# Performance work log

Measured on AMD Instinct MI355X. Metric: run time of the kernel, lower is better.

Reference implementation:

```python
import jax, jax.numpy as jnp
import numpy as np

IGNORE_INDEX = 255
THRESH = 0.7
MIN_KEPT = 100000


def _ohem_ce(predict, target):
    # predict: (n, c, h, w) float logits; target: (n, h, w) int labels
    n, c, h, w = predict.shape
    logits = predict.transpose(0, 2, 3, 1).reshape(-1, c)   # (P, c), P = n*h*w
    labels = target.reshape(-1)                              # (P,)

    valid = labels != IGNORE_INDEX
    safe_labels = jnp.where(valid, labels, 0)

    # stable log-softmax once; prob-at-label = exp(logp-at-label)
    logp = jax.nn.log_softmax(logits, axis=-1)               # (P, c)
    logp_lab = jnp.take_along_axis(logp, safe_labels[:, None], axis=-1)[:, 0]  # (P,)
    pred = jnp.exp(logp_lab)                                 # softmax prob of true class

    num_valid = jnp.sum(valid)

    # k-th smallest prob among valid pixels (selection is not differentiated,
    # matching the torch code which does this on numpy/CPU)
    pred_ng = jax.lax.stop_gradient(pred)
    pred_sel = jnp.where(valid, pred_ng, jnp.inf)
    neg_topk, _ = jax.lax.top_k(-pred_sel, MIN_KEPT)         # MIN_KEPT smallest preds
    kth = -neg_topk[-1]                                      # MIN_KEPT-th smallest

    threshold = jnp.where(kth > THRESH, kth, THRESH)

    # OHEM keep rule only applies when num_valid > min_kept; otherwise keep all valid
    do_ohem = num_valid > MIN_KEPT
    kept = jnp.where(do_ohem, valid & (pred_ng <= threshold), valid)

    cnt = jnp.sum(kept)
    # CrossEntropyLoss(mean over non-ignored) on kept pixels
    loss = -jnp.sum(jnp.where(kept, logp_lab, 0.0)) / jnp.maximum(cnt, 1).astype(logp_lab.dtype)
    return loss


def setup_inputs() -> dict:
    key = jax.random.key(0)
    k1, k2 = jax.random.split(key)
    predict = jax.random.normal(k1, (8, 19, 512, 1024), dtype=jnp.float32)
    target = jax.random.randint(k2, (8, 512, 1024), 0, 19, dtype=jnp.int64)
    return {"predict": predict, "target": target}


def reference(predict, target):
    return _ohem_ce(predict, target)
```

## Files before the change

kernel.cpp:

```cpp
#include <hip/hip_runtime.h>
#include <cfloat>
#include <math.h>

#define P_TOT     4194304
#define HW_       524288
#define NCLS      19
#define IGNORE_IDX 255
#define MIN_KEPT_ 100000
#define NBLK      4096
#define THR       0.7f
#define L2E       1.44269504088896340736f
#define LN2       0.69314718055994530942f

__device__ __forceinline__ double wred_d(double v){
  #pragma unroll
  for (int o = 32; o > 0; o >>= 1) v += __shfl_down(v, o, 64);
  return v;
}
__device__ __forceinline__ unsigned wred_u(unsigned v){
  #pragma unroll
  for (int o = 32; o > 0; o >>= 1) v += __shfl_down(v, o, 64);
  return v;
}

__global__ __launch_bounds__(256) void ohem_pass1(
    const float* __restrict__ logits, const int* __restrict__ tgt,
    double* __restrict__ p_sle, double* __restrict__ p_sva,
    unsigned* __restrict__ p_cnt)
{
  int tid = blockIdx.x * 256 + threadIdx.x;
  int p0  = tid * 4;
  int n   = p0 >> 19;
  int r   = p0 & (HW_ - 1);
  const float* base = logits + (size_t)n * (NCLS * (size_t)HW_) + r;

  int4 tl = *(const int4*)(tgt + p0);
  int q0 = (tl.x != IGNORE_IDX), q1 = (tl.y != IGNORE_IDX);
  int q2 = (tl.z != IGNORE_IDX), q3 = (tl.w != IGNORE_IDX);
  int l0 = q0 ? tl.x : 0, l1 = q1 ? tl.y : 0;
  int l2 = q2 ? tl.z : 0, l3 = q3 ? tl.w : 0;

  float g0 = base[(size_t)l0 * HW_ + 0];
  float g1 = base[(size_t)l1 * HW_ + 1];
  float g2 = base[(size_t)l2 * HW_ + 2];
  float g3 = base[(size_t)l3 * HW_ + 3];

  float4 vals[NCLS];
  float4 mx; mx.x = mx.y = mx.z = mx.w = -FLT_MAX;
  #pragma unroll
  for (int c = 0; c < NCLS; c++){
    float4 v = *(const float4*)(base + (size_t)c * HW_);
    vals[c] = v;
    mx.x = fmaxf(mx.x, v.x); mx.y = fmaxf(mx.y, v.y);
    mx.z = fmaxf(mx.z, v.z); mx.w = fmaxf(mx.w, v.w);
  }
  float4 nm;
  nm.x = -mx.x * L2E; nm.y = -mx.y * L2E;
  nm.z = -mx.z * L2E; nm.w = -mx.w * L2E;
  float4 se; se.x = se.y = se.z = se.w = 0.f;
  #pragma unroll
  for (int c = 0; c < NCLS; c++){
    se.x += exp2f(fmaf(vals[c].x, L2E, nm.x));
    se.y += exp2f(fmaf(vals[c].y, L2E, nm.y));
    se.z += exp2f(fmaf(vals[c].z, L2E, nm.z));
    se.w += exp2f(fmaf(vals[c].w, L2E, nm.w));
  }

  float lp0 = (g0 - mx.x) - log2f(se.x) * LN2;
  float lp1 = (g1 - mx.y) - log2f(se.y) * LN2;
  float lp2 = (g2 - mx.z) - log2f(se.z) * LN2;
  float lp3 = (g3 - mx.w) - log2f(se.w) * LN2;
  float pd0 = __expf(lp0), pd1 = __expf(lp1);
  float pd2 = __expf(lp2), pd3 = __expf(lp3);

  double sle = 0.0, sva = 0.0;
  unsigned cnt = 0;
  #define PIXEL(Q, LP, PD) {                                   \
    if (Q){                                                    \
      cnt += 1u; sva += (double)(LP);                          \
      if ((PD) <= THR){ cnt += 1u << 16; sle += (double)(LP); }\
    }                                                          \
  }
  PIXEL(q0, lp0, pd0) PIXEL(q1, lp1, pd1)
  PIXEL(q2, lp2, pd2) PIXEL(q3, lp3, pd3)
  #undef PIXEL

  sle = wred_d(sle); sva = wred_d(sva); cnt = wred_u(cnt);

  __shared__ double  ls1[4], ls2[4];
  __shared__ unsigned lc[4];
  int wv = threadIdx.x >> 6, ln = threadIdx.x & 63;
  if (ln == 0){ ls1[wv] = sle; ls2[wv] = sva; lc[wv] = cnt; }
  __syncthreads();
  if (threadIdx.x == 0){
    p_sle[blockIdx.x] = ls1[0] + ls1[1] + ls1[2] + ls1[3];
    p_sva[blockIdx.x] = ls2[0] + ls2[1] + ls2[2] + ls2[3];
    p_cnt[blockIdx.x] = lc[0] + lc[1] + lc[2] + lc[3];
  }
}

__global__ __launch_bounds__(1024) void ohem_finish(
    const float* __restrict__ logits, const int* __restrict__ tgt,
    const double* __restrict__ p_sle, const double* __restrict__ p_sva,
    const unsigned* __restrict__ p_cnt,
    unsigned* __restrict__ keys, float* __restrict__ logp,
    float* __restrict__ out)
{
  __shared__ double  rs1[16], rs2[16];
  __shared__ unsigned rc1[16], rc2[16];
  __shared__ unsigned s_flag, s_prefix, s_rank;
  __shared__ unsigned s_hist[4096];

  int t = threadIdx.x;
  double sle = 0.0, sva = 0.0; unsigned cle = 0, cva = 0;
  for (int i = t; i < NBLK; i += 1024){
    sle += p_sle[i]; sva += p_sva[i];
    unsigned c = p_cnt[i];
    cva += c & 0xFFFFu; cle += c >> 16;
  }
  sle = wred_d(sle); sva = wred_d(sva);
  cle = wred_u(cle); cva = wred_u(cva);
  int wv = t >> 6, ln = t & 63;
  if (ln == 0){ rs1[wv] = sle; rs2[wv] = sva; rc1[wv] = cle; rc2[wv] = cva; }
  __syncthreads();
  if (t == 0){
    double S1 = 0, S2 = 0; unsigned C1 = 0, C2 = 0;
    for (int i = 0; i < 16; i++){ S1 += rs1[i]; S2 += rs2[i]; C1 += rc1[i]; C2 += rc2[i]; }
    unsigned flag;
    if (C2 <= MIN_KEPT_){
      unsigned d = C2 > 1u ? C2 : 1u;
      out[0] = (float)(-S2 / (double)d);
      flag = 0;
    } else if (C1 >= MIN_KEPT_){
      out[0] = (float)(-S1 / (double)C1);
      flag = 0;
    } else flag = 1;
    s_flag = flag;
  }
  __syncthreads();
  if (!s_flag) return;

  for (int p = t; p < P_TOT; p += 1024){
    int n = p >> 19; int r = p & (HW_ - 1);
    const float* bp = logits + (size_t)n * (NCLS * (size_t)HW_) + r;
    int lab = tgt[p];
    int lv  = (lab != IGNORE_IDX);
    int ls  = lv ? lab : 0;
    float mxv = -FLT_MAX, va[NCLS];
    #pragma unroll
    for (int c = 0; c < NCLS; c++){
      float x = bp[(size_t)c * HW_];
      va[c] = x; mxv = fmaxf(mxv, x);
    }
    float xlv = va[0];
    #pragma unroll
    for (int c = 1; c < NCLS; c++) if (c == ls) xlv = va[c];
    float sev = 0.f;
    #pragma unroll
    for (int c = 0; c < NCLS; c++) sev += __expf(va[c] - mxv);
    float lp = (xlv - mxv) - __logf(sev);
    float pd = __expf(lp);
    keys[p] = lv ? __float_as_uint(pd) : 0xFFFFFFFFu;
    logp[p] = lp;
  }
  __syncthreads();

  unsigned prefix = 0, rank = MIN_KEPT_;
  #pragma unroll
  for (int rd = 0; rd < 3; rd++){
    const int sh = (rd == 0) ? 20 : (rd == 1) ? 8 : 0;
    const int nb = (rd == 2) ? 8 : 12;
    const unsigned nbin = 1u << nb;
    for (unsigned i = t; i < nbin; i += 1024) s_hist[i] = 0;
    __syncthreads();
    for (int p = t; p < P_TOT; p += 1024){
      unsigned k = keys[p];
      unsigned hi = (rd == 0) ? 0u : (k >> (sh + nb));
      if (hi == prefix) atomicAdd(&s_hist[(k >> sh) & (nbin - 1)], 1u);
    }
    __syncthreads();
    if (t == 0){
      unsigned cum = 0, b = 0;
      for (; b < nbin - 1; b++){
        unsigned cc = s_hist[b];
        if (cum + cc >= rank) break;
        cum += cc;
      }
      s_prefix = (prefix << nb) | b;
      s_rank = rank - cum;
    }
    __syncthreads();
    prefix = s_prefix; rank = s_rank;
    __syncthreads();
  }
  unsigned kb = prefix;

  double s = 0.0; unsigned c = 0;
  for (int p = t; p < P_TOT; p += 1024){
    unsigned k = keys[p];
    if (k <= kb){ c++; s += (double)logp[p]; }
  }
  s = wred_d(s); c = wred_u(c);
  if (ln == 0){ rs1[wv] = s; rc1[wv] = c; }
  __syncthreads();
  if (t == 0){
    double S = 0; unsigned CC = 0;
    for (int i = 0; i < 16; i++){ S += rs1[i]; CC += rc1[i]; }
    unsigned d = CC > 1u ? CC : 1u;
    out[0] = (float)(-S / (double)d);
  }
}

extern "C" void kernel_launch(void* const* d_in, const int* in_sizes, int n_in,
                              void* d_out, int out_size, void* d_ws, size_t ws_size,
                              hipStream_t stream)
{
  const float* logits = (const float*)d_in[0];
  const int*   tgt    = (const int*)d_in[1];
  float* out = (float*)d_out;

  double*   p_sle = (double*)d_ws;
  double*   p_sva = p_sle + NBLK;
  unsigned* p_cnt = (unsigned*)(p_sva + NBLK);
  unsigned* keys  = p_cnt + NBLK;
  float*    logp  = (float*)(keys + P_TOT);

  hipLaunchKernelGGL(ohem_pass1, dim3(NBLK), dim3(256), 0, stream,
                     logits, tgt, p_sle, p_sva, p_cnt);
  hipLaunchKernelGGL(ohem_finish, dim3(1), dim3(1024), 0, stream,
                     logits, tgt, p_sle, p_sva, p_cnt, keys, logp, out);
}
```

Before: 439.3 us.

## Stream logits via double-buffered global_load_lds DMA in persistent single-wave blocks

Pass 1 now launches 1024 single-wave blocks. Each block walks 16 consecutive 256-pixel tiles and prefetches the next tile's 19 class planes and labels into LDS with global_load_lds, double-buffered and ordered by explicit waitcnt. The label-class gather now reads from LDS instead of issuing extra scattered global loads, and the exp/log calls use the raw hardware builtins. The aim is to overlap memory latency with compute on a bandwidth-bound read of about 320MB. The cost is far fewer concurrent waves (1024 wave64s across the GPU), which may not saturate HBM, and the hand-coded waitcnt immediates carry a correctness risk.

```diff
diff --git a/kernel.cpp b/kernel.cpp
--- a/kernel.cpp
+++ b/kernel.cpp
@@ -1,16 +1,26 @@
 #include <hip/hip_runtime.h>
 #include <cfloat>
-#include <math.h>
+#include <stdint.h>
 
 #define P_TOT     4194304
 #define HW_       524288
 #define NCLS      19
 #define IGNORE_IDX 255
 #define MIN_KEPT_ 100000
-#define NBLK      4096
 #define THR       0.7f
 #define L2E       1.44269504088896340736f
 #define LN2       0.69314718055994530942f
+
+#define NWAVE          1024
+#define TILES_PER_WAVE 16
+#define TILE_PX        256
+#define BUF_BYTES      20480
+
+__device__ __forceinline__ void dma16(const void* g, void* l){
+  __builtin_amdgcn_global_load_lds(
+      (const __attribute__((address_space(1))) uint32_t*)g,
+      (__attribute__((address_space(3))) uint32_t*)l, 16, 0, 0);
+}
 
 __device__ __forceinline__ double wred_d(double v){
   #pragma unroll
@@ -23,79 +33,102 @@
   return v;
 }
 
-__global__ __launch_bounds__(256) void ohem_pass1(
+__global__ __launch_bounds__(64) void ohem_pass1(
     const float* __restrict__ logits, const int* __restrict__ tgt,
     double* __restrict__ p_sle, double* __restrict__ p_sva,
     unsigned* __restrict__ p_cnt)
 {
-  int tid = blockIdx.x * 256 + threadIdx.x;
-  int p0  = tid * 4;
-  int n   = p0 >> 19;
-  int r   = p0 & (HW_ - 1);
-  const float* base = logits + (size_t)n * (NCLS * (size_t)HW_) + r;
-
-  int4 tl = *(const int4*)(tgt + p0);
-  int q0 = (tl.x != IGNORE_IDX), q1 = (tl.y != IGNORE_IDX);
-  int q2 = (tl.z != IGNORE_IDX), q3 = (tl.w != IGNORE_IDX);
-  int l0 = q0 ? tl.x : 0, l1 = q1 ? tl.y : 0;
-  int l2 = q2 ? tl.z : 0, l3 = q3 ? tl.w : 0;
-
-  float g0 = base[(size_t)l0 * HW_ + 0];
-  float g1 = base[(size_t)l1 * HW_ + 1];
-  float g2 = base[(size_t)l2 * HW_ + 2];
-  float g3 = base[(size_t)l3 * HW_ + 3];
-
-  float4 vals[NCLS];
-  float4 mx; mx.x = mx.y = mx.z = mx.w = -FLT_MAX;
-  #pragma unroll
-  for (int c = 0; c < NCLS; c++){
-    float4 v = *(const float4*)(base + (size_t)c * HW_);
-    vals[c] = v;
-    mx.x = fmaxf(mx.x, v.x); mx.y = fmaxf(mx.y, v.y);
-    mx.z = fmaxf(mx.z, v.z); mx.w = fmaxf(mx.w, v.w);
-  }
-  float4 nm;
-  nm.x = -mx.x * L2E; nm.y = -mx.y * L2E;
-  nm.z = -mx.z * L2E; nm.w = -mx.w * L2E;
-  float4 se; se.x = se.y = se.z = se.w = 0.f;
-  #pragma unroll
-  for (int c = 0; c < NCLS; c++){
-    se.x += exp2f(fmaf(vals[c].x, L2E, nm.x));
-    se.y += exp2f(fmaf(vals[c].y, L2E, nm.y));
-    se.z += exp2f(fmaf(vals[c].z, L2E, nm.z));
-    se.w += exp2f(fmaf(vals[c].w, L2E, nm.w));
-  }
-
-  float lp0 = (g0 - mx.x) - log2f(se.x) * LN2;
-  float lp1 = (g1 - mx.y) - log2f(se.y) * LN2;
-  float lp2 = (g2 - mx.z) - log2f(se.z) * LN2;
-  float lp3 = (g3 - mx.w) - log2f(se.w) * LN2;
-  float pd0 = __expf(lp0), pd1 = __expf(lp1);
-  float pd2 = __expf(lp2), pd3 = __expf(lp3);
+  __shared__ uint8_t lds[2 * BUF_BYTES];
+  const int lane = threadIdx.x;
+  const int t0   = blockIdx.x * TILES_PER_WAVE;
+
+  {
+    int p0 = t0 * TILE_PX;
+    int n = p0 >> 19, r0 = p0 & (HW_ - 1);
+    const float* pb = logits + (size_t)n * (NCLS * (size_t)HW_) + r0 + lane * 4;
+    #pragma unroll
+    for (int c = 0; c < NCLS; c++)
+      dma16(pb + (size_t)c * HW_, &lds[c * 1024]);
+    dma16(tgt + p0 + lane * 4, &lds[19 * 1024]);
+  }
 
   double sle = 0.0, sva = 0.0;
   unsigned cnt = 0;
-  #define PIXEL(Q, LP, PD) {                                   \
-    if (Q){                                                    \
-      cnt += 1u; sva += (double)(LP);                          \
-      if ((PD) <= THR){ cnt += 1u << 16; sle += (double)(LP); }\
-    }                                                          \
-  }
-  PIXEL(q0, lp0, pd0) PIXEL(q1, lp1, pd1)
-  PIXEL(q2, lp2, pd2) PIXEL(q3, lp3, pd3)
-  #undef PIXEL
+
+  for (int i = 0; i < TILES_PER_WAVE; i++){
+    const uint8_t* buf = &lds[(i & 1) * BUF_BYTES];
+
+    if (i + 1 < TILES_PER_WAVE){
+      int p0 = (t0 + i + 1) * TILE_PX;
+      int n = p0 >> 19, r0 = p0 & (HW_ - 1);
+      const float* pb = logits + (size_t)n * (NCLS * (size_t)HW_) + r0 + lane * 4;
+      uint8_t* nbuf = &lds[((i + 1) & 1) * BUF_BYTES];
+      #pragma unroll
+      for (int c = 0; c < NCLS; c++)
+        dma16(pb + (size_t)c * HW_, nbuf + c * 1024);
+      dma16(tgt + p0 + lane * 4, nbuf + 19 * 1024);
+      __builtin_amdgcn_s_waitcnt(0x4F74);
+    } else {
+      __builtin_amdgcn_s_waitcnt(0x0F70);
+    }
+
+    int4 tl = *((const int4*)(buf + 19 * 1024) + lane);
+
+    float4 vals[NCLS];
+    float4 mx; mx.x = mx.y = mx.z = mx.w = -FLT_MAX;
+    #pragma unroll
+    for (int c = 0; c < NCLS; c++){
+      float4 v = *((const float4*)(buf + c * 1024) + lane);
+      vals[c] = v;
+      mx.x = fmaxf(mx.x, v.x); mx.y = fmaxf(mx.y, v.y);
+      mx.z = fmaxf(mx.z, v.z); mx.w = fmaxf(mx.w, v.w);
+    }
+    float4 nm;
+    nm.x = -mx.x * L2E; nm.y = -mx.y * L2E;
+    nm.z = -mx.z * L2E; nm.w = -mx.w * L2E;
+    float4 se; se.x = se.y = se.z = se.w = 0.f;
+    #pragma unroll
+    for (int c = 0; c < NCLS; c++){
+      se.x += __builtin_amdgcn_exp2f(fmaf(vals[c].x, L2E, nm.x));
+      se.y += __builtin_amdgcn_exp2f(fmaf(vals[c].y, L2E, nm.y));
+      se.z += __builtin_amdgcn_exp2f(fmaf(vals[c].z, L2E, nm.z));
+      se.w += __builtin_amdgcn_exp2f(fmaf(vals[c].w, L2E, nm.w));
+    }
+
+    int q0 = (tl.x != IGNORE_IDX), q1 = (tl.y != IGNORE_IDX);
+    int q2 = (tl.z != IGNORE_IDX), q3 = (tl.w != IGNORE_IDX);
+    int l0 = q0 ? tl.x : 0, l1 = q1 ? tl.y : 0;
+    int l2 = q2 ? tl.z : 0, l3 = q3 ? tl.w : 0;
+    float g0 = *(const float*)(buf + l0 * 1024 + lane * 16 + 0);
+    float g1 = *(const float*)(buf + l1 * 1024 + lane * 16 + 4);
+    float g2 = *(const float*)(buf + l2 * 1024 + lane * 16 + 8);
+    float g3 = *(const float*)(buf + l3 * 1024 + lane * 16 + 12);
+
+    float lp0 = (g0 - mx.x) - __builtin_amdgcn_logf(se.x) * LN2;
+    float lp1 = (g1 - mx.y) - __builtin_amdgcn_logf(se.y) * LN2;
+    float lp2 = (g2 - mx.z) - __builtin_amdgcn_logf(se.z) * LN2;
+    float lp3 = (g3 - mx.w) - __builtin_amdgcn_logf(se.w) * LN2;
+    float pd0 = __builtin_amdgcn_exp2f(lp0 * L2E);
+    float pd1 = __builtin_amdgcn_exp2f(lp1 * L2E);
+    float pd2 = __builtin_amdgcn_exp2f(lp2 * L2E);
+    float pd3 = __builtin_amdgcn_exp2f(lp3 * L2E);
+
+    #define PIXEL(Q, LP, PD) {                                   \
+      if (Q){                                                    \
+        cnt += 1u; sva += (double)(LP);                          \
+        if ((PD) <= THR){ cnt += 1u << 16; sle += (double)(LP); }\
+      }                                                          \
+    }
+    PIXEL(q0, lp0, pd0) PIXEL(q1, lp1, pd1)
+    PIXEL(q2, lp2, pd2) PIXEL(q3, lp3, pd3)
+    #undef PIXEL
+  }
 
   sle = wred_d(sle); sva = wred_d(sva); cnt = wred_u(cnt);
-
-  __shared__ double  ls1[4], ls2[4];
-  __shared__ unsigned lc[4];
-  int wv = threadIdx.x >> 6, ln = threadIdx.x & 63;
-  if (ln == 0){ ls1[wv] = sle; ls2[wv] = sva; lc[wv] = cnt; }
-  __syncthreads();
-  if (threadIdx.x == 0){
-    p_sle[blockIdx.x] = ls1[0] + ls1[1] + ls1[2] + ls1[3];
-    p_sva[blockIdx.x] = ls2[0] + ls2[1] + ls2[2] + ls2[3];
-    p_cnt[blockIdx.x] = lc[0] + lc[1] + lc[2] + lc[3];
+  if (lane == 0){
+    p_sle[blockIdx.x] = sle;
+    p_sva[blockIdx.x] = sva;
+    p_cnt[blockIdx.x] = cnt;
   }
 }
 
@@ -112,12 +145,10 @@
   __shared__ unsigned s_hist[4096];
 
   int t = threadIdx.x;
-  double sle = 0.0, sva = 0.0; unsigned cle = 0, cva = 0;
-  for (int i = t; i < NBLK; i += 1024){
-    sle += p_sle[i]; sva += p_sva[i];
-    unsigned c = p_cnt[i];
-    cva += c & 0xFFFFu; cle += c >> 16;
-  }
+  double sle = p_sle[t], sva = p_sva[t];
+  unsigned c0 = p_cnt[t];
+  unsigned cva = c0 & 0xFFFFu, cle = c0 >> 16;
+
   sle = wred_d(sle); sva = wred_d(sva);
   cle = wred_u(cle); cva = wred_u(cva);
   int wv = t >> 6, ln = t & 63;
@@ -220,12 +251,12 @@
   float* out = (float*)d_out;
 
   double*   p_sle = (double*)d_ws;
-  double*   p_sva = p_sle + NBLK;
-  unsigned* p_cnt = (unsigned*)(p_sva + NBLK);
-  unsigned* keys  = p_cnt + NBLK;
+  double*   p_sva = p_sle + NWAVE;
+  unsigned* p_cnt = (unsigned*)(p_sva + NWAVE);
+  unsigned* keys  = p_cnt + NWAVE;
   float*    logp  = (float*)(keys + P_TOT);
 
-  hipLaunchKernelGGL(ohem_pass1, dim3(NBLK), dim3(256), 0, stream,
+  hipLaunchKernelGGL(ohem_pass1, dim3(NWAVE), dim3(64), 0, stream,
                      logits, tgt, p_sle, p_sva, p_cnt);
   hipLaunchKernelGGL(ohem_finish, dim3(1), dim3(1024), 0, stream,
                      logits, tgt, p_sle, p_sva, p_cnt, keys, logp, out);
```

Result: no change. 441.9 us (+0.6%).

## Restructure OHEM pass1 as per-segment online softmax without label gathers

Applied to the files above, without the earlier changes.

The first pass now gives each 512-thread block a contiguous 8192-pixel segment, with each thread handling 16 pixels. It streams class planes two at a time and uses an online max/sum-exp update. The true-class logit is picked in registers by comparing against the label, which removes the scattered per-pixel gather loads and the 19-entry float4 register array. The costs are more exp2 work per class and fewer blocks in flight, with a non-unrolled class loop limiting memory-level parallelism per thread.

```diff
diff --git a/kernel.cpp b/kernel.cpp
--- a/kernel.cpp
+++ b/kernel.cpp
@@ -1,17 +1,19 @@
 #include <hip/hip_runtime.h>
 #include <cfloat>
-#include <math.h>
+#include <stdint.h>
 
 #define P_TOT     4194304
 #define HW_       524288
 #define NCLS      19
 #define IGNORE_IDX 255
 #define MIN_KEPT_ 100000
-#define NBLK      4096
 #define THR       0.7f
 #define L2E       1.44269504088896340736f
 #define LN2       0.69314718055994530942f
 
+#define SEG_PX    8192
+#define NSEG      512
+
 __device__ __forceinline__ double wred_d(double v){
   #pragma unroll
   for (int o = 32; o > 0; o >>= 1) v += __shfl_down(v, o, 64);
@@ -23,79 +25,90 @@
   return v;
 }
 
-__global__ __launch_bounds__(256) void ohem_pass1(
+__global__ __launch_bounds__(512) void ohem_pass1(
     const float* __restrict__ logits, const int* __restrict__ tgt,
     double* __restrict__ p_sle, double* __restrict__ p_sva,
     unsigned* __restrict__ p_cnt)
 {
-  int tid = blockIdx.x * 256 + threadIdx.x;
-  int p0  = tid * 4;
-  int n   = p0 >> 19;
-  int r   = p0 & (HW_ - 1);
-  const float* base = logits + (size_t)n * (NCLS * (size_t)HW_) + r;
-
-  int4 tl = *(const int4*)(tgt + p0);
-  int q0 = (tl.x != IGNORE_IDX), q1 = (tl.y != IGNORE_IDX);
-  int q2 = (tl.z != IGNORE_IDX), q3 = (tl.w != IGNORE_IDX);
-  int l0 = q0 ? tl.x : 0, l1 = q1 ? tl.y : 0;
-  int l2 = q2 ? tl.z : 0, l3 = q3 ? tl.w : 0;
-
-  float g0 = base[(size_t)l0 * HW_ + 0];
-  float g1 = base[(size_t)l1 * HW_ + 1];
-  float g2 = base[(size_t)l2 * HW_ + 2];
-  float g3 = base[(size_t)l3 * HW_ + 3];
-
-  float4 vals[NCLS];
-  float4 mx; mx.x = mx.y = mx.z = mx.w = -FLT_MAX;
-  #pragma unroll
-  for (int c = 0; c < NCLS; c++){
-    float4 v = *(const float4*)(base + (size_t)c * HW_);
-    vals[c] = v;
-    mx.x = fmaxf(mx.x, v.x); mx.y = fmaxf(mx.y, v.y);
-    mx.z = fmaxf(mx.z, v.z); mx.w = fmaxf(mx.w, v.w);
-  }
-  float4 nm;
-  nm.x = -mx.x * L2E; nm.y = -mx.y * L2E;
-  nm.z = -mx.z * L2E; nm.w = -mx.w * L2E;
-  float4 se; se.x = se.y = se.z = se.w = 0.f;
-  #pragma unroll
-  for (int c = 0; c < NCLS; c++){
-    se.x += exp2f(fmaf(vals[c].x, L2E, nm.x));
-    se.y += exp2f(fmaf(vals[c].y, L2E, nm.y));
-    se.z += exp2f(fmaf(vals[c].z, L2E, nm.z));
-    se.w += exp2f(fmaf(vals[c].w, L2E, nm.w));
-  }
-
-  float lp0 = (g0 - mx.x) - log2f(se.x) * LN2;
-  float lp1 = (g1 - mx.y) - log2f(se.y) * LN2;
-  float lp2 = (g2 - mx.z) - log2f(se.z) * LN2;
-  float lp3 = (g3 - mx.w) - log2f(se.w) * LN2;
-  float pd0 = __expf(lp0), pd1 = __expf(lp1);
-  float pd2 = __expf(lp2), pd3 = __expf(lp3);
-
-  double sle = 0.0, sva = 0.0;
-  unsigned cnt = 0;
-  #define PIXEL(Q, LP, PD) {                                   \
-    if (Q){                                                    \
-      cnt += 1u; sva += (double)(LP);                          \
-      if ((PD) <= THR){ cnt += 1u << 16; sle += (double)(LP); }\
-    }                                                          \
-  }
-  PIXEL(q0, lp0, pd0) PIXEL(q1, lp1, pd1)
-  PIXEL(q2, lp2, pd2) PIXEL(q3, lp3, pd3)
-  #undef PIXEL
-
+  const int t   = threadIdx.x;
+  const int seg = blockIdx.x * SEG_PX;
+  const int n   = seg >> 19;
+  const int r0  = seg & (HW_ - 1);
+  const float* plane0 = logits + (size_t)n * (NCLS * (size_t)HW_) + r0;
+
+  int   lab[16];
+  float m[16], s[16], g[16];
+
+  #pragma unroll
+  for (int j = 0; j < 4; j++){
+    int4 tl = *(const int4*)(tgt + seg + j * 2048 + t * 4);
+    lab[4*j+0] = tl.x; lab[4*j+1] = tl.y; lab[4*j+2] = tl.z; lab[4*j+3] = tl.w;
+  }
+
+  #pragma unroll
+  for (int j = 0; j < 4; j++){
+    float4 v = *(const float4*)(plane0 + j * 2048 + t * 4);
+    float vv[4] = {v.x, v.y, v.z, v.w};
+    #pragma unroll
+    for (int k = 0; k < 4; k++){
+      int p = 4*j + k;
+      m[p] = vv[k]; s[p] = 1.0f;
+      g[p] = (lab[p] == 0) ? vv[k] : 0.0f;
+    }
+  }
+
+  #pragma unroll 1
+  for (int c = 1; c < NCLS; c += 2){
+    const float* pA = plane0 + (size_t)c * HW_;
+    const float* pB = pA + HW_;
+    float4 va[4], vb[4];
+    #pragma unroll
+    for (int j = 0; j < 4; j++){
+      va[j] = *(const float4*)(pA + j * 2048 + t * 4);
+      vb[j] = *(const float4*)(pB + j * 2048 + t * 4);
+    }
+    #pragma unroll
+    for (int j = 0; j < 4; j++){
+      float xa[4] = {va[j].x, va[j].y, va[j].z, va[j].w};
+      float xb[4] = {vb[j].x, vb[j].y, vb[j].z, vb[j].w};
+      #pragma unroll
+      for (int k = 0; k < 4; k++){
+        int p = 4*j + k;
+        float x = xa[k], y = xb[k];
+        float mo = m[p];
+        float mn = fmaxf(mo, fmaxf(x, y));
+        float tt = mn * L2E;
+        s[p] = s[p] * __builtin_amdgcn_exp2f(fmaf(mo, L2E, -tt))
+             + __builtin_amdgcn_exp2f(fmaf(x, L2E, -tt))
+             + __builtin_amdgcn_exp2f(fmaf(y, L2E, -tt));
+        m[p] = mn;
+        g[p] = (lab[p] == c)     ? x : g[p];
+        g[p] = (lab[p] == c + 1) ? y : g[p];
+      }
+    }
+  }
+
+  double sle = 0.0, sva = 0.0; unsigned cnt = 0;
+  #pragma unroll
+  for (int p = 0; p < 16; p++){
+    float lp = (g[p] - m[p]) - __builtin_amdgcn_logf(s[p]) * LN2;
+    float pd = __builtin_amdgcn_exp2f(lp * L2E);
+    if (lab[p] != IGNORE_IDX){
+      cnt += 1u; sva += (double)lp;
+      if (pd <= THR){ cnt += 1u << 16; sle += (double)lp; }
+    }
+  }
   sle = wred_d(sle); sva = wred_d(sva); cnt = wred_u(cnt);
 
-  __shared__ double  ls1[4], ls2[4];
-  __shared__ unsigned lc[4];
-  int wv = threadIdx.x >> 6, ln = threadIdx.x & 63;
-  if (ln == 0){ ls1[wv] = sle; ls2[wv] = sva; lc[wv] = cnt; }
-  __syncthreads();
-  if (threadIdx.x == 0){
-    p_sle[blockIdx.x] = ls1[0] + ls1[1] + ls1[2] + ls1[3];
-    p_sva[blockIdx.x] = ls2[0] + ls2[1] + ls2[2] + ls2[3];
-    p_cnt[blockIdx.x] = lc[0] + lc[1] + lc[2] + lc[3];
+  __shared__ double  ld1[8], ld2[8];
+  __shared__ unsigned lc[8];
+  int wv = t >> 6, ln = t & 63;
+  if (ln == 0){ ld1[wv] = sle; ld2[wv] = sva; lc[wv] = cnt; }
+  __syncthreads();
+  if (t == 0){
+    double a = 0, b = 0; unsigned c2 = 0;
+    for (int i = 0; i < 8; i++){ a += ld1[i]; b += ld2[i]; c2 += lc[i]; }
+    p_sle[blockIdx.x] = a; p_sva[blockIdx.x] = b; p_cnt[blockIdx.x] = c2;
   }
 }
 
@@ -113,7 +126,7 @@
 
   int t = threadIdx.x;
   double sle = 0.0, sva = 0.0; unsigned cle = 0, cva = 0;
-  for (int i = t; i < NBLK; i += 1024){
+  for (int i = t; i < NSEG; i += 1024){
     sle += p_sle[i]; sva += p_sva[i];
     unsigned c = p_cnt[i];
     cva += c & 0xFFFFu; cle += c >> 16;
@@ -220,12 +233,12 @@
   float* out = (float*)d_out;
 
   double*   p_sle = (double*)d_ws;
-  double*   p_sva = p_sle + NBLK;
-  unsigned* p_cnt = (unsigned*)(p_sva + NBLK);
-  unsigned* keys  = p_cnt + NBLK;
+  double*   p_sva = p_sle + NSEG;
+  unsigned* p_cnt = (unsigned*)(p_sva + NSEG);
+  unsigned* keys  = p_cnt + NSEG;
   float*    logp  = (float*)(keys + P_TOT);
 
-  hipLaunchKernelGGL(ohem_pass1, dim3(NBLK), dim3(256), 0, stream,
+  hipLaunchKernelGGL(ohem_pass1, dim3(NSEG), dim3(512), 0, stream,
                      logits, tgt, p_sle, p_sva, p_cnt);
   hipLaunchKernelGGL(ohem_finish, dim3(1), dim3(1024), 0, stream,
                      logits, tgt, p_sle, p_sva, p_cnt, keys, logp, out);
```

Result: faster. 423.1 us (-3.7%).
